# Kernel tuning notes

Hardware: AMD Instinct MI355X
Metric: run time of the kernel (lower is better)

The kernel has to match this reference:

```python
import jax, jax.numpy as jnp
import numpy as np

NUM_HEADS = 16


def setup_inputs() -> dict:
    key = jax.random.key(0)
    ks = jax.random.split(key, 7)
    T, B, E = 2048, 2, 1024
    s = 0.02
    return {
        "query": jax.random.normal(ks[0], (T, B, E), jnp.float32),
        "key": jax.random.normal(ks[1], (T, B, E), jnp.float32),
        "value": jax.random.normal(ks[2], (T, B, E), jnp.float32),
        "in_proj_weight": jax.random.normal(ks[3], (3 * E, E), jnp.float32) * s,
        "in_proj_bias": jax.random.normal(ks[4], (3 * E,), jnp.float32) * s,
        "out_proj_weight": jax.random.normal(ks[5], (E, E), jnp.float32) * s,
        "out_proj_bias": jax.random.normal(ks[6], (E,), jnp.float32) * s,
    }


def reference(query, key, value, in_proj_weight, in_proj_bias,
              out_proj_weight, out_proj_bias):
    T, B, E = query.shape
    H = NUM_HEADS
    Dh = E // H
    Wq, Wk, Wv = jnp.split(in_proj_weight, 3, axis=0)   # each (E, E)
    bq, bk, bv = jnp.split(in_proj_bias, 3, axis=0)
    # packed in-projection (F._in_projection_packed)
    q = query @ Wq.T + bq   # (T, B, E)
    k = key @ Wk.T + bk
    v = value @ Wv.T + bv
    # (T, B, E) -> (B, H, T, Dh)
    def to_heads(x):
        return x.reshape(T, B, H, Dh).transpose(1, 2, 0, 3)
    q, k, v = to_heads(q), to_heads(k), to_heads(v)
    scale = 1.0 / jnp.sqrt(jnp.asarray(Dh, q.dtype))
    scores = jnp.einsum('bhtd,bhsd->bhts', q, k) * scale  # (B, H, T, T)
    attn = jax.nn.softmax(scores, axis=-1)
    ctx = jnp.einsum('bhts,bhsd->bhtd', attn, v)          # (B, H, T, Dh)
    # (B, H, T, Dh) -> (T, B, E)
    ctx = ctx.transpose(2, 0, 1, 3).reshape(T, B, E)
    out = ctx @ out_proj_weight.T + out_proj_bias          # (T, B, E)
    return out
```

## Files before the change

kernel.cpp:

```cpp
#include <hip/hip_runtime.h>
#include <stdint.h>


typedef __bf16 bf16;
typedef __bf16 bf16x8 __attribute__((ext_vector_type(8)));
typedef float f32x4 __attribute__((ext_vector_type(4)));
typedef unsigned int u32x4 __attribute__((ext_vector_type(4)));

#define MFMA16(a, b, c) __builtin_amdgcn_mfma_f32_16x16x32_bf16((a), (b), (c), 0, 0, 0)

static __device__ __forceinline__ void gload_lds16(const void* g, void* lds) {
  __builtin_amdgcn_global_load_lds(
      (__attribute__((address_space(1))) void*)(g),
      (__attribute__((address_space(3))) void*)(lds), 16u, 0, 0u);
}

static __device__ __forceinline__ unsigned pack2_bf16(float a, float b) {
  unsigned short ua = __builtin_bit_cast(unsigned short, (bf16)a);
  unsigned short ub = __builtin_bit_cast(unsigned short, (bf16)b);
  return (unsigned)ua | ((unsigned)ub << 16);
}

__global__ __launch_bounds__(256) void cvt5_kernel(
    const float* __restrict__ s0, const float* __restrict__ s1,
    const float* __restrict__ s2, const float* __restrict__ s3,
    const float* __restrict__ s4,
    bf16* __restrict__ d0, bf16* __restrict__ d1, bf16* __restrict__ d2,
    bf16* __restrict__ d3, bf16* __restrict__ d4) {
  const int y = blockIdx.y;
  const float* s; bf16* d; int n8;
  switch (y) {
    case 0: s = s0; d = d0; n8 = 524288; break;
    case 1: s = s1; d = d1; n8 = 524288; break;
    case 2: s = s2; d = d2; n8 = 524288; break;
    case 3: s = s3; d = d3; n8 = 393216; break;
    default: s = s4; d = d4; n8 = 131072; break;
  }
  const int i = blockIdx.x * 256 + threadIdx.x;
  if (i >= n8) return;
  const float4* sp = reinterpret_cast<const float4*>(s) + (size_t)i * 2;
  float4 a = sp[0], b = sp[1];
  bf16x8 o;
  o[0] = (bf16)a.x; o[1] = (bf16)a.y; o[2] = (bf16)a.z; o[3] = (bf16)a.w;
  o[4] = (bf16)b.x; o[5] = (bf16)b.y; o[6] = (bf16)b.z; o[7] = (bf16)b.w;
  *reinterpret_cast<bf16x8*>(d + (size_t)i * 8) = o;
}

static __device__ __forceinline__ void gemm_tile_compute(
    const bf16* Ab, const bf16* Bb, int wm, int wn, int g, int c15,
    f32x4 (&acc)[4][4]) {
  bf16x8 af[4], bfr[4];
#pragma unroll
  for (int mi = 0; mi < 4; ++mi)
    af[mi] = *reinterpret_cast<const bf16x8*>(Ab + (((wm * 4 + mi) * 4 + g) * 16 + c15) * 8);
#pragma unroll
  for (int ni = 0; ni < 4; ++ni)
    bfr[ni] = *reinterpret_cast<const bf16x8*>(Bb + (((wn * 4 + ni) * 4 + g) * 16 + c15) * 8);
#pragma unroll
  for (int mi = 0; mi < 4; ++mi)
#pragma unroll
    for (int ni = 0; ni < 4; ++ni)
      acc[mi][ni] = MFMA16(af[mi], bfr[ni], acc[mi][ni]);
}

static __device__ __forceinline__ void gemm_core_128x128(
    const bf16* __restrict__ A, const bf16* __restrict__ Bw, int K,
    bf16* Alds, bf16* Blds, f32x4 (&acc)[4][4]) {
  const int tid = threadIdx.x;
  const int wid = tid >> 6, lane = tid & 63;
  const int g = lane >> 4, c15 = lane & 15;
  const int wm = wid >> 1, wn = wid & 1;
#pragma unroll
  for (int mi = 0; mi < 4; ++mi)
#pragma unroll
    for (int ni = 0; ni < 4; ++ni) acc[mi][ni] = f32x4{0.f, 0.f, 0.f, 0.f};

  const int u0 = tid, u1 = 256 + tid;
  const int row0 = ((u0 >> 6) << 4) + (u0 & 15), col0 = ((u0 >> 4) & 3) * 8;
  const int row1 = ((u1 >> 6) << 4) + (u1 & 15), col1 = ((u1 >> 4) & 3) * 8;
  const bf16* ga0 = A + (size_t)row0 * K + col0;
  const bf16* ga1 = A + (size_t)row1 * K + col1;
  const bf16* gb0 = Bw + (size_t)row0 * K + col0;
  const bf16* gb1 = Bw + (size_t)row1 * K + col1;
  const int lofs0 = wid * 512, lofs1 = 2048 + wid * 512;

#define GSTAGE(kt, buf) do {                                   \
    gload_lds16(ga0 + (kt), Alds + (buf) * 4096 + lofs0);      \
    gload_lds16(ga1 + (kt), Alds + (buf) * 4096 + lofs1);      \
    gload_lds16(gb0 + (kt), Blds + (buf) * 4096 + lofs0);      \
    gload_lds16(gb1 + (kt), Blds + (buf) * 4096 + lofs1);      \
  } while (0)

  GSTAGE(0, 0);
  __syncthreads();
  int cur = 0;
  for (int kt = 32; kt < K; kt += 32) {
    GSTAGE(kt, cur ^ 1);
    gemm_tile_compute(Alds + cur * 4096, Blds + cur * 4096, wm, wn, g, c15, acc);
    __syncthreads();
    cur ^= 1;
  }
  gemm_tile_compute(Alds + cur * 4096, Blds + cur * 4096, wm, wn, g, c15, acc);
#undef GSTAGE
}

__global__ __launch_bounds__(256) void gemm_inproj(
    const bf16* __restrict__ xq, const bf16* __restrict__ xk, const bf16* __restrict__ xv,
    const bf16* __restrict__ w, const float* __restrict__ bias,
    bf16* __restrict__ qo, bf16* __restrict__ ko, bf16* __restrict__ vto) {
  __shared__ __align__(16) bf16 Alds[2 * 4096];
  __shared__ __align__(16) bf16 Blds[2 * 4096];
  const int m0 = blockIdx.x * 128, n0 = blockIdx.y * 128;
  const int tensor = n0 >> 10;
  const bf16* A = (tensor == 0 ? xq : tensor == 1 ? xk : xv) + (size_t)m0 * 1024;
  const bf16* Bw = w + (size_t)n0 * 1024;
  f32x4 acc[4][4];
  gemm_core_128x128(A, Bw, 1024, Alds, Blds, acc);

  const int lane = threadIdx.x & 63, wid = threadIdx.x >> 6;
  const int g = lane >> 4, c15 = lane & 15;
  const int wm = wid >> 1, wn = wid & 1;
  const float QS = 0.18033688011112042f;
#pragma unroll
  for (int mi = 0; mi < 4; ++mi)
#pragma unroll
    for (int ni = 0; ni < 4; ++ni) {
      const int n = n0 + wn * 64 + ni * 16 + c15;
      const float bn = bias[n];
      const int h = (n >> 6) & 15, d = n & 63;
#pragma unroll
      for (int r = 0; r < 4; ++r) {
        const int m = m0 + wm * 64 + mi * 16 + 4 * g + r;
        const int t = m >> 1, b = m & 1;
        const int bh = b * 16 + h;
        const float v = acc[mi][ni][r] + bn;
        if (tensor == 0)
          qo[((size_t)bh * 2048 + t) * 64 + d] = (bf16)(v * QS);
        else if (tensor == 1)
          ko[((size_t)bh * 2048 + t) * 64 + d] = (bf16)v;
        else
          vto[((size_t)bh * 64 + d) * 2048 + t] = (bf16)v;
      }
    }
}

__global__ __launch_bounds__(256) void gemm_outproj(
    const bf16* __restrict__ ctx, const bf16* __restrict__ w,
    const float* __restrict__ bias, float* __restrict__ out) {
  __shared__ __align__(16) bf16 Alds[2 * 4096];
  __shared__ __align__(16) bf16 Blds[2 * 4096];
  const int m0 = blockIdx.x * 128, n0 = blockIdx.y * 128;
  f32x4 acc[4][4];
  gemm_core_128x128(ctx + (size_t)m0 * 1024, w + (size_t)n0 * 1024, 1024, Alds, Blds, acc);

  const int lane = threadIdx.x & 63, wid = threadIdx.x >> 6;
  const int g = lane >> 4, c15 = lane & 15;
  const int wm = wid >> 1, wn = wid & 1;
#pragma unroll
  for (int mi = 0; mi < 4; ++mi)
#pragma unroll
    for (int ni = 0; ni < 4; ++ni) {
      const int n = n0 + wn * 64 + ni * 16 + c15;
      const float bn = bias[n];
#pragma unroll
      for (int r = 0; r < 4; ++r) {
        const int m = m0 + wm * 64 + mi * 16 + 4 * g + r;
        out[(size_t)m * 1024 + n] = acc[mi][ni][r] + bn;
      }
    }
}

__global__ __launch_bounds__(256) void attn_kernel(
    const bf16* __restrict__ q, const bf16* __restrict__ k,
    const bf16* __restrict__ vt, bf16* __restrict__ ctx) {
  __shared__ __align__(16) bf16 Klds[2 * 4096];
  __shared__ __align__(16) bf16 Vlds[2 * 4096];
  const int tid = threadIdx.x;
  const int wid = tid >> 6, lane = tid & 63;
  const int g = lane >> 4, c15 = lane & 15;
  const int bh = blockIdx.y;
  const int q0 = blockIdx.x * 64;
  const size_t headoff = (size_t)bh * 2048 * 64;

  const bf16* qrow = q + headoff + (size_t)(q0 + wid * 16 + c15) * 64;
  const bf16x8 qf0 = *reinterpret_cast<const bf16x8*>(qrow + 8 * g);
  const bf16x8 qf1 = *reinterpret_cast<const bf16x8*>(qrow + 32 + 8 * g);

  f32x4 acc[4];
#pragma unroll
  for (int i = 0; i < 4; ++i) acc[i] = f32x4{0.f, 0.f, 0.f, 0.f};
  float lsum[4] = {0.f, 0.f, 0.f, 0.f};

  const int u0 = tid, u1 = 256 + tid;
  const int row0 = ((u0 >> 7) << 4) + (u0 & 15), col0 = ((u0 >> 6) & 1) * 32 + ((u0 >> 4) & 3) * 8;
  const int row1 = ((u1 >> 7) << 4) + (u1 & 15), col1 = ((u1 >> 6) & 1) * 32 + ((u1 >> 4) & 3) * 8;
  const bf16* kbase = k + headoff;
  const bf16* vbase = vt + headoff;
  const int lofs0 = wid * 512, lofs1 = 2048 + wid * 512;
  const int ghi = (g >> 1) & 1;

#define ASTAGE(kt, buf) do {                                                        \
    const int kv0_ = (kt) * 64;                                                     \
    gload_lds16(kbase + (size_t)(kv0_ + row0) * 64 + col0, Klds + (buf) * 4096 + lofs0); \
    gload_lds16(kbase + (size_t)(kv0_ + row1) * 64 + col1, Klds + (buf) * 4096 + lofs1); \
    gload_lds16(vbase + (size_t)row0 * 2048 + kv0_ + col0, Vlds + (buf) * 4096 + lofs0); \
    gload_lds16(vbase + (size_t)row1 * 2048 + kv0_ + col1, Vlds + (buf) * 4096 + lofs1); \
  } while (0)

  ASTAGE(0, 0);
  __syncthreads();
  int cur = 0;

  for (int kt = 0; kt < 32; ++kt) {
    if (kt < 31) ASTAGE(kt + 1, cur ^ 1);
    const bf16* Kb = Klds + cur * 4096;
    const bf16* Vb = Vlds + cur * 4096;

    f32x4 sc[4];
#pragma unroll
    for (int c = 0; c < 4; ++c) {
      const bf16x8 kf0 = *reinterpret_cast<const bf16x8*>(Kb + (((c * 2 + 0) * 4 + g) * 16 + c15) * 8);
      const bf16x8 kf1 = *reinterpret_cast<const bf16x8*>(Kb + (((c * 2 + 1) * 4 + g) * 16 + c15) * 8);
      f32x4 s = f32x4{0.f, 0.f, 0.f, 0.f};
      s = MFMA16(kf0, qf0, s);
      s = MFMA16(kf1, qf1, s);
      sc[c] = s;
    }

    float p[4][4];
#pragma unroll
    for (int c = 0; c < 4; ++c) {
      float ps = 0.f;
#pragma unroll
      for (int r = 0; r < 4; ++r) {
        p[c][r] = __builtin_amdgcn_exp2f(sc[c][r]);
        ps += p[c][r];
      }
      lsum[c] += ps;
    }

    unsigned pk[4][2];
#pragma unroll
    for (int c = 0; c < 4; ++c) {
      pk[c][0] = pack2_bf16(p[c][0], p[c][1]);
      pk[c][1] = pack2_bf16(p[c][2], p[c][3]);
    }
    u32x4 pvu[2];
#pragma unroll
    for (int kkv = 0; kkv < 2; ++kkv) {
      unsigned wrec[2][2];
#pragma unroll
      for (int u = 0; u < 2; ++u)
#pragma unroll
        for (int v = 0; v < 2; ++v) {
          const unsigned val = ((g & 1) ^ u) ? pk[kkv * 2 + 1][v] : pk[kkv * 2][v];
          wrec[u][v] = __shfl(val, ((g & 1) * 2 + ((g >> 1) ^ u)) * 16 + c15);
        }
      pvu[kkv][0] = ghi ? wrec[1][0] : wrec[0][0];
      pvu[kkv][1] = ghi ? wrec[1][1] : wrec[0][1];
      pvu[kkv][2] = ghi ? wrec[0][0] : wrec[1][0];
      pvu[kkv][3] = ghi ? wrec[0][1] : wrec[1][1];
    }
    const bf16x8 pvf0 = __builtin_bit_cast(bf16x8, pvu[0]);
    const bf16x8 pvf1 = __builtin_bit_cast(bf16x8, pvu[1]);

#pragma unroll
    for (int dc = 0; dc < 4; ++dc) {
      const bf16x8 vf0 = *reinterpret_cast<const bf16x8*>(Vb + (((dc * 2 + 0) * 4 + g) * 16 + c15) * 8);
      const bf16x8 vf1 = *reinterpret_cast<const bf16x8*>(Vb + (((dc * 2 + 1) * 4 + g) * 16 + c15) * 8);
      acc[dc] = MFMA16(vf0, pvf0, acc[dc]);
      acc[dc] = MFMA16(vf1, pvf1, acc[dc]);
    }

    __syncthreads();
    cur ^= 1;
  }
#undef ASTAGE

  float l = (lsum[0] + lsum[1]) + (lsum[2] + lsum[3]);
  l += __shfl_xor(l, 16);
  l += __shfl_xor(l, 32);
  const float rinv = 1.0f / l;
  const int t = q0 + wid * 16 + c15;
  const int b = bh >> 4, h = bh & 15;
  bf16* cbase = ctx + (size_t)(t * 2 + b) * 1024 + h * 64;
#pragma unroll
  for (int dc = 0; dc < 4; ++dc)
#pragma unroll
    for (int r = 0; r < 4; ++r)
      cbase[dc * 16 + 4 * g + r] = (bf16)(acc[dc][r] * rinv);
}

extern "C" void kernel_launch(void* const* d_in, const int* in_sizes, int n_in,
                              void* d_out, int out_size, void* d_ws, size_t ws_size,
                              hipStream_t stream) {
  const float* query = (const float*)d_in[0];
  const float* key   = (const float*)d_in[1];
  const float* value = (const float*)d_in[2];
  const float* in_w  = (const float*)d_in[3];
  const float* in_b  = (const float*)d_in[4];
  const float* out_w = (const float*)d_in[5];
  const float* out_b = (const float*)d_in[6];

  bf16* ws = (bf16*)d_ws;
  const size_t M4 = 4194304;
  bf16* xq  = ws;
  bf16* xk  = xq + M4;
  bf16* xv  = xk + M4;
  bf16* wi  = xv + M4;
  bf16* wo  = wi + 3145728;
  bf16* qh  = wo + 1048576;
  bf16* kh  = qh + M4;
  bf16* vth = kh + M4;
  bf16* ctx = vth + M4;

  cvt5_kernel<<<dim3(2048, 5), 256, 0, stream>>>(query, key, value, in_w, out_w,
                                                 xq, xk, xv, wi, wo);
  gemm_inproj<<<dim3(32, 24), 256, 0, stream>>>(xq, xk, xv, wi, in_b, qh, kh, vth);
  attn_kernel<<<dim3(32, 32), 256, 0, stream>>>(qh, kh, vth, ctx);
  gemm_outproj<<<dim3(32, 8), 256, 0, stream>>>(ctx, wo, out_b, (float*)d_out);
}
```

Before: 265.2 us.

## Process 32 query rows per wave and compute row sums via MFMA

Each wave now handles two 16-row query tiles, so every K/V tile loaded into LDS is reused across 128 queries per block instead of 64, halving the grid. The softmax denominator is now computed with an MFMA against a vector of ones (on the bf16-rounded probabilities) rather than scalar adds plus cross-lane shuffles. Launch bounds request 2 blocks per CU. This raises register pressure and halves the block count, which could hurt occupancy or load balance.

```diff
diff --git a/kernel.cpp b/kernel.cpp
--- a/kernel.cpp
+++ b/kernel.cpp
@@ -170,7 +170,42 @@
     }
 }
 
-__global__ __launch_bounds__(256) void attn_kernel(
+static __device__ __forceinline__ void softmax_dist(
+    const f32x4 (&sc)[4], int g, int c15, int ghi,
+    bf16x8& pvf0, bf16x8& pvf1) {
+  float p[4][4];
+#pragma unroll
+  for (int c = 0; c < 4; ++c)
+#pragma unroll
+    for (int r = 0; r < 4; ++r) p[c][r] = __builtin_amdgcn_exp2f(sc[c][r]);
+
+  unsigned pk[4][2];
+#pragma unroll
+  for (int c = 0; c < 4; ++c) {
+    pk[c][0] = pack2_bf16(p[c][0], p[c][1]);
+    pk[c][1] = pack2_bf16(p[c][2], p[c][3]);
+  }
+  u32x4 pvu[2];
+#pragma unroll
+  for (int kkv = 0; kkv < 2; ++kkv) {
+    unsigned wrec[2][2];
+#pragma unroll
+    for (int u = 0; u < 2; ++u)
+#pragma unroll
+      for (int v = 0; v < 2; ++v) {
+        const unsigned val = ((g & 1) ^ u) ? pk[kkv * 2 + 1][v] : pk[kkv * 2][v];
+        wrec[u][v] = __shfl(val, ((g & 1) * 2 + ((g >> 1) ^ u)) * 16 + c15);
+      }
+    pvu[kkv][0] = ghi ? wrec[1][0] : wrec[0][0];
+    pvu[kkv][1] = ghi ? wrec[1][1] : wrec[0][1];
+    pvu[kkv][2] = ghi ? wrec[0][0] : wrec[1][0];
+    pvu[kkv][3] = ghi ? wrec[0][1] : wrec[1][1];
+  }
+  pvf0 = __builtin_bit_cast(bf16x8, pvu[0]);
+  pvf1 = __builtin_bit_cast(bf16x8, pvu[1]);
+}
+
+__global__ __launch_bounds__(256, 2) void attn_kernel(
     const bf16* __restrict__ q, const bf16* __restrict__ k,
     const bf16* __restrict__ vt, bf16* __restrict__ ctx) {
   __shared__ __align__(16) bf16 Klds[2 * 4096];
@@ -178,18 +213,29 @@
   const int tid = threadIdx.x;
   const int wid = tid >> 6, lane = tid & 63;
   const int g = lane >> 4, c15 = lane & 15;
+  const int ghi = (g >> 1) & 1;
   const int bh = blockIdx.y;
-  const int q0 = blockIdx.x * 64;
+  const int q0 = blockIdx.x * 128;
   const size_t headoff = (size_t)bh * 2048 * 64;
 
-  const bf16* qrow = q + headoff + (size_t)(q0 + wid * 16 + c15) * 64;
-  const bf16x8 qf0 = *reinterpret_cast<const bf16x8*>(qrow + 8 * g);
-  const bf16x8 qf1 = *reinterpret_cast<const bf16x8*>(qrow + 32 + 8 * g);
-
-  f32x4 acc[4];
-#pragma unroll
-  for (int i = 0; i < 4; ++i) acc[i] = f32x4{0.f, 0.f, 0.f, 0.f};
-  float lsum[4] = {0.f, 0.f, 0.f, 0.f};
+  const bf16* qrow0 = q + headoff + (size_t)(q0 + wid * 32 + c15) * 64;
+  const bf16* qrow1 = qrow0 + 16 * 64;
+  const bf16x8 qf0a = *reinterpret_cast<const bf16x8*>(qrow0 + 8 * g);
+  const bf16x8 qf0b = *reinterpret_cast<const bf16x8*>(qrow0 + 32 + 8 * g);
+  const bf16x8 qf1a = *reinterpret_cast<const bf16x8*>(qrow1 + 8 * g);
+  const bf16x8 qf1b = *reinterpret_cast<const bf16x8*>(qrow1 + 32 + 8 * g);
+
+  f32x4 acc0[4], acc1[4], accl0, accl1;
+#pragma unroll
+  for (int i = 0; i < 4; ++i) {
+    acc0[i] = f32x4{0.f, 0.f, 0.f, 0.f};
+    acc1[i] = f32x4{0.f, 0.f, 0.f, 0.f};
+  }
+  accl0 = f32x4{0.f, 0.f, 0.f, 0.f};
+  accl1 = f32x4{0.f, 0.f, 0.f, 0.f};
+  bf16x8 ones;
+#pragma unroll
+  for (int j = 0; j < 8; ++j) ones[j] = (bf16)1.0f;
 
   const int u0 = tid, u1 = 256 + tid;
   const int row0 = ((u0 >> 7) << 4) + (u0 & 15), col0 = ((u0 >> 6) & 1) * 32 + ((u0 >> 4) & 3) * 8;
@@ -197,7 +243,6 @@
   const bf16* kbase = k + headoff;
   const bf16* vbase = vt + headoff;
   const int lofs0 = wid * 512, lofs1 = 2048 + wid * 512;
-  const int ghi = (g >> 1) & 1;
 
 #define ASTAGE(kt, buf) do {                                                        \
     const int kv0_ = (kt) * 64;                                                     \
@@ -216,79 +261,55 @@
     const bf16* Kb = Klds + cur * 4096;
     const bf16* Vb = Vlds + cur * 4096;
 
-    f32x4 sc[4];
+    f32x4 sc0[4], sc1[4];
 #pragma unroll
     for (int c = 0; c < 4; ++c) {
       const bf16x8 kf0 = *reinterpret_cast<const bf16x8*>(Kb + (((c * 2 + 0) * 4 + g) * 16 + c15) * 8);
       const bf16x8 kf1 = *reinterpret_cast<const bf16x8*>(Kb + (((c * 2 + 1) * 4 + g) * 16 + c15) * 8);
-      f32x4 s = f32x4{0.f, 0.f, 0.f, 0.f};
-      s = MFMA16(kf0, qf0, s);
-      s = MFMA16(kf1, qf1, s);
-      sc[c] = s;
+      const f32x4 z = f32x4{0.f, 0.f, 0.f, 0.f};
+      sc0[c] = MFMA16(kf1, qf0b, MFMA16(kf0, qf0a, z));
+      sc1[c] = MFMA16(kf1, qf1b, MFMA16(kf0, qf1a, z));
     }
 
-    float p[4][4];
-#pragma unroll
-    for (int c = 0; c < 4; ++c) {
-      float ps = 0.f;
-#pragma unroll
-      for (int r = 0; r < 4; ++r) {
-        p[c][r] = __builtin_amdgcn_exp2f(sc[c][r]);
-        ps += p[c][r];
-      }
-      lsum[c] += ps;
-    }
-
-    unsigned pk[4][2];
-#pragma unroll
-    for (int c = 0; c < 4; ++c) {
-      pk[c][0] = pack2_bf16(p[c][0], p[c][1]);
-      pk[c][1] = pack2_bf16(p[c][2], p[c][3]);
-    }
-    u32x4 pvu[2];
-#pragma unroll
-    for (int kkv = 0; kkv < 2; ++kkv) {
-      unsigned wrec[2][2];
-#pragma unroll
-      for (int u = 0; u < 2; ++u)
-#pragma unroll
-        for (int v = 0; v < 2; ++v) {
-          const unsigned val = ((g & 1) ^ u) ? pk[kkv * 2 + 1][v] : pk[kkv * 2][v];
-          wrec[u][v] = __shfl(val, ((g & 1) * 2 + ((g >> 1) ^ u)) * 16 + c15);
-        }
-      pvu[kkv][0] = ghi ? wrec[1][0] : wrec[0][0];
-      pvu[kkv][1] = ghi ? wrec[1][1] : wrec[0][1];
-      pvu[kkv][2] = ghi ? wrec[0][0] : wrec[1][0];
-      pvu[kkv][3] = ghi ? wrec[0][1] : wrec[1][1];
-    }
-    const bf16x8 pvf0 = __builtin_bit_cast(bf16x8, pvu[0]);
-    const bf16x8 pvf1 = __builtin_bit_cast(bf16x8, pvu[1]);
+    bf16x8 pa0, pb0, pa1, pb1;
+    softmax_dist(sc0, g, c15, ghi, pa0, pb0);
+    softmax_dist(sc1, g, c15, ghi, pa1, pb1);
 
 #pragma unroll
     for (int dc = 0; dc < 4; ++dc) {
       const bf16x8 vf0 = *reinterpret_cast<const bf16x8*>(Vb + (((dc * 2 + 0) * 4 + g) * 16 + c15) * 8);
       const bf16x8 vf1 = *reinterpret_cast<const bf16x8*>(Vb + (((dc * 2 + 1) * 4 + g) * 16 + c15) * 8);
-      acc[dc] = MFMA16(vf0, pvf0, acc[dc]);
-      acc[dc] = MFMA16(vf1, pvf1, acc[dc]);
+      acc0[dc] = MFMA16(vf1, pb0, MFMA16(vf0, pa0, acc0[dc]));
+      acc1[dc] = MFMA16(vf1, pb1, MFMA16(vf0, pa1, acc1[dc]));
     }
+    accl0 = MFMA16(ones, pb0, MFMA16(ones, pa0, accl0));
+    accl1 = MFMA16(ones, pb1, MFMA16(ones, pa1, accl1));
 
     __syncthreads();
     cur ^= 1;
   }
 #undef ASTAGE
 
-  float l = (lsum[0] + lsum[1]) + (lsum[2] + lsum[3]);
-  l += __shfl_xor(l, 16);
-  l += __shfl_xor(l, 32);
-  const float rinv = 1.0f / l;
-  const int t = q0 + wid * 16 + c15;
   const int b = bh >> 4, h = bh & 15;
-  bf16* cbase = ctx + (size_t)(t * 2 + b) * 1024 + h * 64;
-#pragma unroll
-  for (int dc = 0; dc < 4; ++dc)
-#pragma unroll
-    for (int r = 0; r < 4; ++r)
-      cbase[dc * 16 + 4 * g + r] = (bf16)(acc[dc][r] * rinv);
+  const int t0 = q0 + wid * 32 + c15;
+  {
+    const float rinv = 1.0f / accl0[0];
+    bf16* cbase = ctx + (size_t)(t0 * 2 + b) * 1024 + h * 64;
+#pragma unroll
+    for (int dc = 0; dc < 4; ++dc)
+#pragma unroll
+      for (int r = 0; r < 4; ++r)
+        cbase[dc * 16 + 4 * g + r] = (bf16)(acc0[dc][r] * rinv);
+  }
+  {
+    const float rinv = 1.0f / accl1[0];
+    bf16* cbase = ctx + (size_t)((t0 + 16) * 2 + b) * 1024 + h * 64;
+#pragma unroll
+    for (int dc = 0; dc < 4; ++dc)
+#pragma unroll
+      for (int r = 0; r < 4; ++r)
+        cbase[dc * 16 + 4 * g + r] = (bf16)(acc1[dc][r] * rinv);
+  }
 }
 
 extern "C" void kernel_launch(void* const* d_in, const int* in_sizes, int n_in,
@@ -317,6 +338,6 @@
   cvt5_kernel<<<dim3(2048, 5), 256, 0, stream>>>(query, key, value, in_w, out_w,
                                                  xq, xk, xv, wi, wo);
   gemm_inproj<<<dim3(32, 24), 256, 0, stream>>>(xq, xk, xv, wi, in_b, qh, kh, vth);
-  attn_kernel<<<dim3(32, 32), 256, 0, stream>>>(qh, kh, vth, ctx);
+  attn_kernel<<<dim3(16, 32), 256, 0, stream>>>(qh, kh, vth, ctx);
   gemm_outproj<<<dim3(32, 8), 256, 0, stream>>>(ctx, wo, out_b, (float*)d_out);
 }
```

Measured after the change: 259.8 us. -2.1%, faster.
